# Performance work log

Measured on AMD Instinct MI355X. Metric: run time of the kernel, lower is better.

## Reference

```python
import jax, jax.numpy as jnp
import numpy as np
import math

D_MODEL = 1024
NUM_HEADS = 16
N_GROUP = 4
HEAD_DIM = D_MODEL // NUM_HEADS  # 64
KV_DIM = N_GROUP * HEAD_DIM      # 256
BS, SEQ = 2, 2048


def setup_inputs() -> dict:
    key = jax.random.key(0)
    ks = jax.random.split(key, 7)
    s = 0.02
    return {
        "h": jax.random.normal(ks[0], (BS, SEQ, D_MODEL), dtype=jnp.float32),
        "wq_w": jax.random.normal(ks[1], (D_MODEL, D_MODEL), dtype=jnp.float32) * s,
        "wq_b": jnp.zeros((D_MODEL,), dtype=jnp.float32),
        "wk_w": jax.random.normal(ks[2], (KV_DIM, D_MODEL), dtype=jnp.float32) * s,
        "wk_b": jnp.zeros((KV_DIM,), dtype=jnp.float32),
        "wv_w": jax.random.normal(ks[3], (KV_DIM, D_MODEL), dtype=jnp.float32) * s,
        "wv_b": jnp.zeros((KV_DIM,), dtype=jnp.float32),
    }


def reference(h, wq_w, wq_b, wk_w, wk_b, wv_w, wv_b):
    bs, seq, _ = h.shape
    rep = NUM_HEADS // N_GROUP  # heads per KV group

    # Linear projections (torch Linear: x @ W.T + b)
    q = h @ wq_w.T + wq_b                     # [bs, seq, d_model]
    k = h @ wk_w.T + wk_b                     # [bs, seq, kv_dim]
    v = h @ wv_w.T + wv_b                     # [bs, seq, kv_dim]

    q = q.reshape(bs, seq, NUM_HEADS, HEAD_DIM).transpose(0, 2, 1, 3)  # [b,H,s,d]
    k = k.reshape(bs, seq, N_GROUP, HEAD_DIM)                          # [b,s,G,d]
    v = v.reshape(bs, seq, N_GROUP, HEAD_DIM)
    # torch .repeat(1,1,1,rep).view(...,num_heads,head_dim) maps head h -> group h//rep,
    # identical to repeating each group `rep` times consecutively along the head axis.
    k = jnp.repeat(k, rep, axis=2).transpose(0, 2, 1, 3)               # [b,H,s,d]
    v = jnp.repeat(v, rep, axis=2).transpose(0, 2, 1, 3)               # [b,H,s,d]

    scores = jnp.einsum("bhqd,bhkd->bhqk", q, k) / math.sqrt(HEAD_DIM)
    attn = jax.nn.softmax(scores, axis=-1)
    out = jnp.einsum("bhqk,bhkd->bhqd", attn, v)                       # [b,H,s,d]
    out = out.transpose(0, 2, 1, 3).reshape(bs, seq, NUM_HEADS * HEAD_DIM)
    return out
```

## Files before the change

kernel.cpp:

```cpp
#include <hip/hip_runtime.h>

typedef _Float16 f16;
typedef _Float16 f16x8 __attribute__((ext_vector_type(8)));
typedef _Float16 f16x4 __attribute__((ext_vector_type(4)));
typedef float f32x4 __attribute__((ext_vector_type(4)));

#define MFMA16(a, b, c) __builtin_amdgcn_mfma_f32_16x16x32_f16((a), (b), (c), 0, 0, 0)

#define SEQ 2048
#define DMODEL 1024
#define NH 16
#define NG 4
#define PAD 76

__device__ __forceinline__ f16x8 cvt8(const float4 a, const float4 b) {
    f16x8 r;
    r[0] = (f16)a.x; r[1] = (f16)a.y; r[2] = (f16)a.z; r[3] = (f16)a.w;
    r[4] = (f16)b.x; r[5] = (f16)b.y; r[6] = (f16)b.z; r[7] = (f16)b.w;
    return r;
}

__global__ __launch_bounds__(256) void qkv_gemm(const float* __restrict__ hA,
                                                const float* __restrict__ wq,
                                                const float* __restrict__ wk,
                                                const float* __restrict__ wv,
                                                const float* __restrict__ bq,
                                                const float* __restrict__ bk,
                                                const float* __restrict__ bv,
                                                f16* __restrict__ Qb,
                                                f16* __restrict__ Kb,
                                                f16* __restrict__ Vtb,
                                                float qscale) {
    __shared__ __align__(16) f16 As[128 * 32];
    __shared__ __align__(16) f16 Bs[128 * 32];

    const int tid  = threadIdx.x;
    const int lane = tid & 63;
    const int l15  = lane & 15;
    const int l4   = lane >> 4;
    const int wave = tid >> 6;
    const int wm   = (wave >> 1) * 64;
    const int wn   = (wave & 1) * 64;
    const int bx   = blockIdx.x;
    const int m0   = blockIdx.y * 128;

    const float* W; const float* bias; f16* C; int N, n0; float osc; int vmode;
    if (bx < 8)       { W = wq; bias = bq; C = Qb;  N = 1024; n0 = bx * 128;        osc = qscale; vmode = 0; }
    else if (bx < 10) { W = wk; bias = bk; C = Kb;  N = 256;  n0 = (bx - 8) * 128;  osc = 1.0f;   vmode = 0; }
    else              { W = wv; bias = bv; C = Vtb; N = 256;  n0 = (bx - 10) * 128; osc = 1.0f;   vmode = 1; }

    const int rowT = tid >> 2;
    const int colT = (tid & 3) * 8;
    const float* Ag = hA + (size_t)(m0 + rowT) * DMODEL + colT;
    const float* Bg = W  + (size_t)(n0 + rowT) * DMODEL + colT;

    f32x4 acc[4][4];
#pragma unroll
    for (int i = 0; i < 4; i++)
#pragma unroll
        for (int j = 0; j < 4; j++) acc[i][j] = (f32x4)0.0f;

    float4 ra[4], rb[4];
    ra[0] = *(const float4*)(Ag);
    ra[1] = *(const float4*)(Ag + 4);
    ra[2] = *(const float4*)(Ag + (size_t)64 * DMODEL);
    ra[3] = *(const float4*)(Ag + (size_t)64 * DMODEL + 4);
    rb[0] = *(const float4*)(Bg);
    rb[1] = *(const float4*)(Bg + 4);
    rb[2] = *(const float4*)(Bg + (size_t)64 * DMODEL);
    rb[3] = *(const float4*)(Bg + (size_t)64 * DMODEL + 4);

    for (int k0 = 0; k0 < DMODEL; k0 += 32) {
        __syncthreads();
        *(f16x8*)&As[rowT * 32 + colT]        = cvt8(ra[0], ra[1]);
        *(f16x8*)&As[(rowT + 64) * 32 + colT] = cvt8(ra[2], ra[3]);
        *(f16x8*)&Bs[rowT * 32 + colT]        = cvt8(rb[0], rb[1]);
        *(f16x8*)&Bs[(rowT + 64) * 32 + colT] = cvt8(rb[2], rb[3]);
        if (k0 + 32 < DMODEL) {
            const int kn = k0 + 32;
            ra[0] = *(const float4*)(Ag + kn);
            ra[1] = *(const float4*)(Ag + kn + 4);
            ra[2] = *(const float4*)(Ag + (size_t)64 * DMODEL + kn);
            ra[3] = *(const float4*)(Ag + (size_t)64 * DMODEL + kn + 4);
            rb[0] = *(const float4*)(Bg + kn);
            rb[1] = *(const float4*)(Bg + kn + 4);
            rb[2] = *(const float4*)(Bg + (size_t)64 * DMODEL + kn);
            rb[3] = *(const float4*)(Bg + (size_t)64 * DMODEL + kn + 4);
        }
        __syncthreads();

        f16x8 af[4], bf[4];
#pragma unroll
        for (int i = 0; i < 4; i++)
            af[i] = *(const f16x8*)&As[(wm + i * 16 + l15) * 32 + l4 * 8];
#pragma unroll
        for (int j = 0; j < 4; j++)
            bf[j] = *(const f16x8*)&Bs[(wn + j * 16 + l15) * 32 + l4 * 8];
#pragma unroll
        for (int i = 0; i < 4; i++)
#pragma unroll
            for (int j = 0; j < 4; j++)
                acc[i][j] = MFMA16(af[i], bf[j], acc[i][j]);
    }

#pragma unroll
    for (int i = 0; i < 4; i++) {
        const int mbase = m0 + wm + i * 16 + l4 * 4;
#pragma unroll
        for (int j = 0; j < 4; j++) {
            const int n  = n0 + wn + j * 16 + l15;
            const float bv = bias[n];
            if (vmode == 0) {
#pragma unroll
                for (int r = 0; r < 4; r++)
                    C[(size_t)(mbase + r) * N + n] = (f16)((acc[i][j][r] + bv) * osc);
            } else {
                f16x4 p;
#pragma unroll
                for (int r = 0; r < 4; r++)
                    p[r] = (f16)((acc[i][j][r] + bv) * osc);
                const int bb = mbase >> 11;
                const int s  = mbase & 2047;
                *(f16x4*)&C[((size_t)(bb * 256 + n)) * SEQ + s] = p;
            }
        }
    }
}

__global__ __launch_bounds__(256, 4) void attn_kernel(const f16* __restrict__ Q,
                                                      const f16* __restrict__ Kt,
                                                      const f16* __restrict__ Vt,
                                                      float* __restrict__ out) {
    __shared__ __align__(16) f16 Ks[64 * PAD];
    __shared__ __align__(16) f16 Vs[64 * PAD];
    __shared__ __align__(16) f16 Ps[64 * PAD];

    const int tid  = threadIdx.x;
    const int lane = tid & 63;
    const int l15  = lane & 15;
    const int l4   = lane >> 4;
    const int wave = tid >> 6;
    const int b    = blockIdx.z;
    const int hh   = blockIdx.y;
    const int g    = hh >> 2;
    const int q0   = blockIdx.x * 64;
    const int qw   = wave * 16;

    f16x8 qf[2];
#pragma unroll
    for (int kt = 0; kt < 2; kt++)
        qf[kt] = *(const f16x8*)&Q[((size_t)(b * SEQ + q0 + qw + l15)) * DMODEL + hh * 64 + kt * 32 + l4 * 8];

    f32x4 oacc[4];
    float lsum[4];
#pragma unroll
    for (int dt = 0; dt < 4; dt++) oacc[dt] = (f32x4)0.0f;
#pragma unroll
    for (int r = 0; r < 4; r++) lsum[r] = 0.0f;

    const int srow = tid >> 2;
    const int sc8  = (tid & 3) * 8;
    const f16* Kg = Kt + (size_t)(b * SEQ + srow) * 256 + g * 64 + sc8;
    const f16* Vg = Vt + (size_t)(b * 256 + g * 64 + srow) * SEQ + sc8;

    for (int kb = 0; kb < SEQ; kb += 64) {
        *(f16x8*)&Ks[srow * PAD + sc8]      = *(const f16x8*)(Kg + (size_t)kb * 256);
        *(f16x8*)&Ks[srow * PAD + 32 + sc8] = *(const f16x8*)(Kg + (size_t)kb * 256 + 32);
        *(f16x8*)&Vs[srow * PAD + sc8]      = *(const f16x8*)(Vg + kb);
        *(f16x8*)&Vs[srow * PAD + 32 + sc8] = *(const f16x8*)(Vg + kb + 32);
        __syncthreads();

        f32x4 sacc[4];
#pragma unroll
        for (int jt = 0; jt < 4; jt++) sacc[jt] = (f32x4)0.0f;
#pragma unroll
        for (int jt = 0; jt < 4; jt++) {
            const f16x8 kf0 = *(const f16x8*)&Ks[(jt * 16 + l15) * PAD + l4 * 8];
            const f16x8 kf1 = *(const f16x8*)&Ks[(jt * 16 + l15) * PAD + 32 + l4 * 8];
            sacc[jt] = MFMA16(qf[0], kf0, sacc[jt]);
            sacc[jt] = MFMA16(qf[1], kf1, sacc[jt]);
        }

#pragma unroll
        for (int jt = 0; jt < 4; jt++)
#pragma unroll
            for (int r = 0; r < 4; r++) {
                const float p = exp2f(fminf(sacc[jt][r], 14.0f));
                lsum[r] += p;
                Ps[(qw + l4 * 4 + r) * PAD + jt * 16 + l15] = (f16)p;
            }

#pragma unroll
        for (int kt = 0; kt < 2; kt++) {
            const f16x8 pf = *(const f16x8*)&Ps[(qw + l15) * PAD + kt * 32 + l4 * 8];
#pragma unroll
            for (int dt = 0; dt < 4; dt++) {
                const f16x8 vf = *(const f16x8*)&Vs[(dt * 16 + l15) * PAD + kt * 32 + l4 * 8];
                oacc[dt] = MFMA16(pf, vf, oacc[dt]);
            }
        }
        __syncthreads();
    }

#pragma unroll
    for (int r = 0; r < 4; r++) {
        float l = lsum[r];
        l += __shfl_xor(l, 1);
        l += __shfl_xor(l, 2);
        l += __shfl_xor(l, 4);
        l += __shfl_xor(l, 8);
        const float inv = 1.0f / l;
        const int q = q0 + qw + l4 * 4 + r;
        float* op = out + ((size_t)(b * SEQ + q)) * DMODEL + hh * 64;
#pragma unroll
        for (int dt = 0; dt < 4; dt++)
            op[dt * 16 + l15] = oacc[dt][r] * inv;
    }
}

extern "C" void kernel_launch(void* const* d_in, const int* in_sizes, int n_in,
                              void* d_out, int out_size, void* d_ws, size_t ws_size,
                              hipStream_t stream) {
    const float* h    = (const float*)d_in[0];
    const float* wq_w = (const float*)d_in[1];
    const float* wq_b = (const float*)d_in[2];
    const float* wk_w = (const float*)d_in[3];
    const float* wk_b = (const float*)d_in[4];
    const float* wv_w = (const float*)d_in[5];
    const float* wv_b = (const float*)d_in[6];
    float* out = (float*)d_out;

    char* ws = (char*)d_ws;
    f16* Qb  = (f16*)(ws + 0);
    f16* Kb  = (f16*)(ws + 8388608);
    f16* Vtb = (f16*)(ws + 10485760);

    const float qscale = 0.125f * 1.4426950408889634f;
    qkv_gemm<<<dim3(12, 32), 256, 0, stream>>>(h, wq_w, wk_w, wv_w, wq_b, wk_b, wv_b,
                                               Qb, Kb, Vtb, qscale);

    attn_kernel<<<dim3(32, 16, 2), 256, 0, stream>>>(Qb, Kb, Vtb, out);
}
```

Measured before the change: 187.7 us.

## Double GEMM K-tile to 64, pad shared memory, remap blocks for L2 locality

The QKV projection GEMM now stages 64-wide K slices per iteration instead of 32. This halves the number of barrier pairs per tile and doubles the register prefetch depth. Shared-memory rows are padded to 72 halves to reduce LDS bank conflicts on the fragment reads. The grid is flattened to 1D with a swizzled block-to-tile mapping so that concurrently running blocks share A rows and weight tiles in L2/LLC. The cost is more registers and more shared memory per block, which may reduce occupancy.

```diff
diff --git a/kernel.cpp b/kernel.cpp
--- a/kernel.cpp
+++ b/kernel.cpp
@@ -12,6 +12,7 @@
 #define NH 16
 #define NG 4
 #define PAD 76
+#define QPAD 72
 
 __device__ __forceinline__ f16x8 cvt8(const float4 a, const float4 b) {
     f16x8 r;
@@ -31,8 +32,8 @@
                                                 f16* __restrict__ Kb,
                                                 f16* __restrict__ Vtb,
                                                 float qscale) {
-    __shared__ __align__(16) f16 As[128 * 32];
-    __shared__ __align__(16) f16 Bs[128 * 32];
+    __shared__ __align__(16) f16 As[128 * QPAD];
+    __shared__ __align__(16) f16 Bs[128 * QPAD];
 
     const int tid  = threadIdx.x;
     const int lane = tid & 63;
@@ -41,16 +42,19 @@
     const int wave = tid >> 6;
     const int wm   = (wave >> 1) * 64;
     const int wn   = (wave & 1) * 64;
-    const int bx   = blockIdx.x;
-    const int m0   = blockIdx.y * 128;
+
+    const int bid = blockIdx.x;
+    const int my  = (bid & 7) * 4 + ((bid >> 3) & 3);
+    const int bx  = bid >> 5;
+    const int m0  = my * 128;
 
     const float* W; const float* bias; f16* C; int N, n0; float osc; int vmode;
     if (bx < 8)       { W = wq; bias = bq; C = Qb;  N = 1024; n0 = bx * 128;        osc = qscale; vmode = 0; }
     else if (bx < 10) { W = wk; bias = bk; C = Kb;  N = 256;  n0 = (bx - 8) * 128;  osc = 1.0f;   vmode = 0; }
     else              { W = wv; bias = bv; C = Vtb; N = 256;  n0 = (bx - 10) * 128; osc = 1.0f;   vmode = 1; }
 
-    const int rowT = tid >> 2;
-    const int colT = (tid & 3) * 8;
+    const int rowT = tid >> 1;
+    const int colT = (tid & 1) * 32;
     const float* Ag = hA + (size_t)(m0 + rowT) * DMODEL + colT;
     const float* Bg = W  + (size_t)(n0 + rowT) * DMODEL + colT;
 
@@ -60,47 +64,45 @@
 #pragma unroll
         for (int j = 0; j < 4; j++) acc[i][j] = (f32x4)0.0f;
 
-    float4 ra[4], rb[4];
-    ra[0] = *(const float4*)(Ag);
-    ra[1] = *(const float4*)(Ag + 4);
-    ra[2] = *(const float4*)(Ag + (size_t)64 * DMODEL);
-    ra[3] = *(const float4*)(Ag + (size_t)64 * DMODEL + 4);
-    rb[0] = *(const float4*)(Bg);
-    rb[1] = *(const float4*)(Bg + 4);
-    rb[2] = *(const float4*)(Bg + (size_t)64 * DMODEL);
-    rb[3] = *(const float4*)(Bg + (size_t)64 * DMODEL + 4);
-
-    for (int k0 = 0; k0 < DMODEL; k0 += 32) {
-        __syncthreads();
-        *(f16x8*)&As[rowT * 32 + colT]        = cvt8(ra[0], ra[1]);
-        *(f16x8*)&As[(rowT + 64) * 32 + colT] = cvt8(ra[2], ra[3]);
-        *(f16x8*)&Bs[rowT * 32 + colT]        = cvt8(rb[0], rb[1]);
-        *(f16x8*)&Bs[(rowT + 64) * 32 + colT] = cvt8(rb[2], rb[3]);
-        if (k0 + 32 < DMODEL) {
-            const int kn = k0 + 32;
-            ra[0] = *(const float4*)(Ag + kn);
-            ra[1] = *(const float4*)(Ag + kn + 4);
-            ra[2] = *(const float4*)(Ag + (size_t)64 * DMODEL + kn);
-            ra[3] = *(const float4*)(Ag + (size_t)64 * DMODEL + kn + 4);
-            rb[0] = *(const float4*)(Bg + kn);
-            rb[1] = *(const float4*)(Bg + kn + 4);
-            rb[2] = *(const float4*)(Bg + (size_t)64 * DMODEL + kn);
-            rb[3] = *(const float4*)(Bg + (size_t)64 * DMODEL + kn + 4);
-        }
-        __syncthreads();
-
-        f16x8 af[4], bf[4];
-#pragma unroll
-        for (int i = 0; i < 4; i++)
-            af[i] = *(const f16x8*)&As[(wm + i * 16 + l15) * 32 + l4 * 8];
-#pragma unroll
-        for (int j = 0; j < 4; j++)
-            bf[j] = *(const f16x8*)&Bs[(wn + j * 16 + l15) * 32 + l4 * 8];
-#pragma unroll
-        for (int i = 0; i < 4; i++)
+    float4 ra[8], rb[8];
+#pragma unroll
+    for (int c = 0; c < 8; c++) {
+        ra[c] = *(const float4*)(Ag + c * 4);
+        rb[c] = *(const float4*)(Bg + c * 4);
+    }
+
+    for (int k0 = 0; k0 < DMODEL; k0 += 64) {
+        __syncthreads();
+#pragma unroll
+        for (int c = 0; c < 4; c++) {
+            *(f16x8*)&As[rowT * QPAD + colT + c * 8] = cvt8(ra[2 * c], ra[2 * c + 1]);
+            *(f16x8*)&Bs[rowT * QPAD + colT + c * 8] = cvt8(rb[2 * c], rb[2 * c + 1]);
+        }
+        if (k0 + 64 < DMODEL) {
+            const int kn = k0 + 64;
+#pragma unroll
+            for (int c = 0; c < 8; c++) {
+                ra[c] = *(const float4*)(Ag + kn + c * 4);
+                rb[c] = *(const float4*)(Bg + kn + c * 4);
+            }
+        }
+        __syncthreads();
+
+#pragma unroll
+        for (int kc = 0; kc < 2; kc++) {
+            f16x8 af[4], bf[4];
+#pragma unroll
+            for (int i = 0; i < 4; i++)
+                af[i] = *(const f16x8*)&As[(wm + i * 16 + l15) * QPAD + kc * 32 + l4 * 8];
 #pragma unroll
             for (int j = 0; j < 4; j++)
-                acc[i][j] = MFMA16(af[i], bf[j], acc[i][j]);
+                bf[j] = *(const f16x8*)&Bs[(wn + j * 16 + l15) * QPAD + kc * 32 + l4 * 8];
+#pragma unroll
+            for (int i = 0; i < 4; i++)
+#pragma unroll
+                for (int j = 0; j < 4; j++)
+                    acc[i][j] = MFMA16(af[i], bf[j], acc[i][j]);
+        }
     }
 
 #pragma unroll
@@ -236,8 +238,8 @@
     f16* Vtb = (f16*)(ws + 10485760);
 
     const float qscale = 0.125f * 1.4426950408889634f;
-    qkv_gemm<<<dim3(12, 32), 256, 0, stream>>>(h, wq_w, wk_w, wv_w, wq_b, wk_b, wv_b,
-                                               Qb, Kb, Vtb, qscale);
+    qkv_gemm<<<dim3(384), 256, 0, stream>>>(h, wq_w, wk_w, wv_w, wq_b, wk_b, wv_b,
+                                            Qb, Kb, Vtb, qscale);
 
     attn_kernel<<<dim3(32, 16, 2), 256, 0, stream>>>(Qb, Kb, Vtb, out);
 }
```

Measured after the change: 225.0 us. 19.9% more time.

## Split attention KV range in two with a combine kernel, reuse K smem for P

Applied to the files above, without the earlier changes.

Splits each attention block's key range into two halves on separate blocks, doubling the grid, and writes unnormalized partial outputs and row sums to workspace. A new combine kernel sums the partials and normalizes. Shared memory for P now reuses the K buffer, with an extra barrier, and launch bounds rise to 8 blocks per CU for more occupancy. The exp clamp is removed, which trades a small amount of ALU work for overflow risk. The extra 32MB partial-output round trip through memory and a third kernel launch are added costs.

```diff
diff --git a/kernel.cpp b/kernel.cpp
--- a/kernel.cpp
+++ b/kernel.cpp
@@ -127,20 +127,22 @@
     }
 }
 
-__global__ __launch_bounds__(256, 4) void attn_kernel(const f16* __restrict__ Q,
+__global__ __launch_bounds__(256, 8) void attn_kernel(const f16* __restrict__ Q,
                                                       const f16* __restrict__ Kt,
                                                       const f16* __restrict__ Vt,
-                                                      float* __restrict__ out) {
-    __shared__ __align__(16) f16 Ks[64 * PAD];
+                                                      float* __restrict__ Op,
+                                                      float* __restrict__ Lp) {
+    __shared__ __align__(16) f16 KPs[64 * PAD];
     __shared__ __align__(16) f16 Vs[64 * PAD];
-    __shared__ __align__(16) f16 Ps[64 * PAD];
 
     const int tid  = threadIdx.x;
     const int lane = tid & 63;
     const int l15  = lane & 15;
     const int l4   = lane >> 4;
     const int wave = tid >> 6;
-    const int b    = blockIdx.z;
+    const int bz   = blockIdx.z;
+    const int b    = bz >> 1;
+    const int sp   = bz & 1;
     const int hh   = blockIdx.y;
     const int g    = hh >> 2;
     const int q0   = blockIdx.x * 64;
@@ -163,11 +165,12 @@
     const f16* Kg = Kt + (size_t)(b * SEQ + srow) * 256 + g * 64 + sc8;
     const f16* Vg = Vt + (size_t)(b * 256 + g * 64 + srow) * SEQ + sc8;
 
-    for (int kb = 0; kb < SEQ; kb += 64) {
-        *(f16x8*)&Ks[srow * PAD + sc8]      = *(const f16x8*)(Kg + (size_t)kb * 256);
-        *(f16x8*)&Ks[srow * PAD + 32 + sc8] = *(const f16x8*)(Kg + (size_t)kb * 256 + 32);
-        *(f16x8*)&Vs[srow * PAD + sc8]      = *(const f16x8*)(Vg + kb);
-        *(f16x8*)&Vs[srow * PAD + 32 + sc8] = *(const f16x8*)(Vg + kb + 32);
+    const int kb0 = sp * (SEQ / 2);
+    for (int kb = kb0; kb < kb0 + SEQ / 2; kb += 64) {
+        *(f16x8*)&KPs[srow * PAD + sc8]      = *(const f16x8*)(Kg + (size_t)kb * 256);
+        *(f16x8*)&KPs[srow * PAD + 32 + sc8] = *(const f16x8*)(Kg + (size_t)kb * 256 + 32);
+        *(f16x8*)&Vs[srow * PAD + sc8]       = *(const f16x8*)(Vg + kb);
+        *(f16x8*)&Vs[srow * PAD + 32 + sc8]  = *(const f16x8*)(Vg + kb + 32);
         __syncthreads();
 
         f32x4 sacc[4];
@@ -175,24 +178,25 @@
         for (int jt = 0; jt < 4; jt++) sacc[jt] = (f32x4)0.0f;
 #pragma unroll
         for (int jt = 0; jt < 4; jt++) {
-            const f16x8 kf0 = *(const f16x8*)&Ks[(jt * 16 + l15) * PAD + l4 * 8];
-            const f16x8 kf1 = *(const f16x8*)&Ks[(jt * 16 + l15) * PAD + 32 + l4 * 8];
+            const f16x8 kf0 = *(const f16x8*)&KPs[(jt * 16 + l15) * PAD + l4 * 8];
+            const f16x8 kf1 = *(const f16x8*)&KPs[(jt * 16 + l15) * PAD + 32 + l4 * 8];
             sacc[jt] = MFMA16(qf[0], kf0, sacc[jt]);
             sacc[jt] = MFMA16(qf[1], kf1, sacc[jt]);
         }
+        __syncthreads();
 
 #pragma unroll
         for (int jt = 0; jt < 4; jt++)
 #pragma unroll
             for (int r = 0; r < 4; r++) {
-                const float p = exp2f(fminf(sacc[jt][r], 14.0f));
+                const float p = exp2f(sacc[jt][r]);
                 lsum[r] += p;
-                Ps[(qw + l4 * 4 + r) * PAD + jt * 16 + l15] = (f16)p;
+                KPs[(qw + l4 * 4 + r) * PAD + jt * 16 + l15] = (f16)p;
             }
 
 #pragma unroll
         for (int kt = 0; kt < 2; kt++) {
-            const f16x8 pf = *(const f16x8*)&Ps[(qw + l15) * PAD + kt * 32 + l4 * 8];
+            const f16x8 pf = *(const f16x8*)&KPs[(qw + l15) * PAD + kt * 32 + l4 * 8];
 #pragma unroll
             for (int dt = 0; dt < 4; dt++) {
                 const f16x8 vf = *(const f16x8*)&Vs[(dt * 16 + l15) * PAD + kt * 32 + l4 * 8];
@@ -209,13 +213,30 @@
         l += __shfl_xor(l, 2);
         l += __shfl_xor(l, 4);
         l += __shfl_xor(l, 8);
-        const float inv = 1.0f / l;
         const int q = q0 + qw + l4 * 4 + r;
-        float* op = out + ((size_t)(b * SEQ + q)) * DMODEL + hh * 64;
+        float* op = Op + (size_t)sp * 4194304 + ((size_t)(b * SEQ + q)) * DMODEL + hh * 64;
 #pragma unroll
         for (int dt = 0; dt < 4; dt++)
-            op[dt * 16 + l15] = oacc[dt][r] * inv;
-    }
+            op[dt * 16 + l15] = oacc[dt][r];
+        if (l15 == 0)
+            Lp[sp * 65536 + (b * SEQ + q) * NH + hh] = l;
+    }
+}
+
+__global__ __launch_bounds__(256) void combine(const float* __restrict__ Op,
+                                               const float* __restrict__ Lp,
+                                               float* __restrict__ out) {
+    const int i = blockIdx.x * 256 + threadIdx.x;
+    const float4 o0 = ((const float4*)Op)[i];
+    const float4 o1 = ((const float4*)(Op + 4194304))[i];
+    const int bqh = i >> 4;
+    const float inv = 1.0f / (Lp[bqh] + Lp[65536 + bqh]);
+    float4 r;
+    r.x = (o0.x + o1.x) * inv;
+    r.y = (o0.y + o1.y) * inv;
+    r.z = (o0.z + o1.z) * inv;
+    r.w = (o0.w + o1.w) * inv;
+    ((float4*)out)[i] = r;
 }
 
 extern "C" void kernel_launch(void* const* d_in, const int* in_sizes, int n_in,
@@ -231,13 +252,17 @@
     float* out = (float*)d_out;
 
     char* ws = (char*)d_ws;
-    f16* Qb  = (f16*)(ws + 0);
-    f16* Kb  = (f16*)(ws + 8388608);
-    f16* Vtb = (f16*)(ws + 10485760);
+    f16*   Qb  = (f16*)(ws + 0);
+    f16*   Kb  = (f16*)(ws + 8388608);
+    f16*   Vtb = (f16*)(ws + 10485760);
+    float* Opb = (float*)(ws + 12582912);
+    float* Lpb = (float*)(ws + 46137344);
 
     const float qscale = 0.125f * 1.4426950408889634f;
     qkv_gemm<<<dim3(12, 32), 256, 0, stream>>>(h, wq_w, wk_w, wv_w, wq_b, wk_b, wv_b,
                                                Qb, Kb, Vtb, qscale);
 
-    attn_kernel<<<dim3(32, 16, 2), 256, 0, stream>>>(Qb, Kb, Vtb, out);
-}
+    attn_kernel<<<dim3(32, 16, 4), 256, 0, stream>>>(Qb, Kb, Vtb, Opb, Lpb);
+
+    combine<<<dim3(4096), 256, 0, stream>>>(Opb, Lpb, out);
+}
```

Measured after the change: 204.1 us. +8.7%, slower.
